# Kernel optimization log

Hardware: AMD Instinct MI355X
Metric: run time of the kernel (lower is better)

Reference implementation:

```python
import jax, jax.numpy as jnp
import numpy as np

B, T, D, H = 4096, 512, 8, 64  # batch, seq_len, input_size, hidden_size


def setup_inputs() -> dict:
    key = jax.random.key(0)
    ks = jax.random.split(key, 11)
    s = lambda k, shape: (jax.random.normal(k, shape, dtype=jnp.float32) * 0.1)
    return {
        "x": jax.random.normal(ks[0], (B, T, D), dtype=jnp.float32),
        # layer 0 (input_size -> H), PyTorch gate order i,f,g,o packed along 4H
        "Wih0": s(ks[1], (4 * H, D)),
        "Whh0": s(ks[2], (4 * H, H)),
        "bih0": s(ks[3], (4 * H,)),
        "bhh0": s(ks[4], (4 * H,)),
        # layer 1 (H -> H)
        "Wih1": s(ks[5], (4 * H, H)),
        "Whh1": s(ks[6], (4 * H, H)),
        "bih1": s(ks[7], (4 * H,)),
        "bhh1": s(ks[8], (4 * H,)),
        # final linear head H -> 1
        "Wfc": s(ks[9], (1, H)),
        "bfc": s(ks[10], (1,)),
    }


def _lstm_layer(x, Wih, Whh, bih, bhh):
    """Single-direction LSTM layer over x:[B,T,Din] -> hs:[B,T,H]."""
    b, t, _ = x.shape
    h_dim = Whh.shape[1]
    # Precompute input contribution for all timesteps (one big GEMM).
    xg = jnp.einsum("btd,gd->btg", x, Wih) + bih + bhh  # [B,T,4H]

    def step(carry, gx_t):
        h, c = carry
        z = gx_t + h @ Whh.T  # [B,4H]
        i, f, g, o = jnp.split(z, 4, axis=-1)
        i = jax.nn.sigmoid(i)
        f = jax.nn.sigmoid(f)
        g = jnp.tanh(g)
        o = jax.nn.sigmoid(o)
        c = f * c + i * g
        h = o * jnp.tanh(c)
        return (h, c), h

    h0 = jnp.zeros((b, h_dim), x.dtype)
    c0 = jnp.zeros((b, h_dim), x.dtype)
    (_, _), hs = jax.lax.scan(step, (h0, c0), jnp.swapaxes(xg, 0, 1))
    return jnp.swapaxes(hs, 0, 1)  # [B,T,H]


def reference(x, Wih0, Whh0, bih0, bhh0, Wih1, Whh1, bih1, bhh1, Wfc, bfc):
    # nn.LSTM with num_layers=2, batch_first=True; dropout inactive in eval.
    h1 = _lstm_layer(x, Wih0, Whh0, bih0, bhh0)
    h2 = _lstm_layer(h1, Wih1, Whh1, bih1, bhh1)
    last = h2[:, -1, :]  # [B,H]
    return last @ Wfc.T + bfc  # [B,1]
```

## Files before the change

### kernel.cpp

```cpp
#include <hip/hip_runtime.h>

#define BTOT 4096
#define TB   512
#define BD   8
#define BSL  16

#define A0TOG  2048
#define A1BASE 4096
#define A1TOG  1024
#define XBASE  6144
#define XTOG   8192
#define NLDS   22528

typedef __attribute__((ext_vector_type(8))) short  short8;
typedef __attribute__((ext_vector_type(4))) float  f32x4;

static __device__ __forceinline__ unsigned short f2bf(float f) {
    unsigned u = __float_as_uint(f);
    u += 0x7fffu + ((u >> 16) & 1u);
    return (unsigned short)(u >> 16);
}
static __device__ __forceinline__ float bf2f(unsigned short h) {
    return __uint_as_float(((unsigned)h) << 16);
}
static __device__ __forceinline__ unsigned pkbf(float a, float b) {
    unsigned r;
    asm("v_cvt_pk_bf16_f32 %0, %1, %2" : "=v"(r) : "v"(a), "v"(b));
    return r;
}

static __device__ __forceinline__ void inv8(const float d[8], float v[8]) {
    const float p0 = d[0]*d[1], p1 = d[2]*d[3], p2 = d[4]*d[5], p3 = d[6]*d[7];
    const float q0 = p0*p1, q1 = p2*p3;
    const float r  = __builtin_amdgcn_rcpf(q0*q1);
    const float iq0 = q1*r,  iq1 = q0*r;
    const float ip0 = p1*iq0, ip1 = p0*iq0, ip2 = p3*iq1, ip3 = p2*iq1;
    v[0]=d[1]*ip0; v[1]=d[0]*ip0; v[2]=d[3]*ip1; v[3]=d[2]*ip1;
    v[4]=d[5]*ip2; v[5]=d[4]*ip2; v[6]=d[7]*ip3; v[7]=d[6]*ip3;
}
static __device__ __forceinline__ void inv4(const float d[4], float v[4]) {
    const float p0 = d[0]*d[1], p1 = d[2]*d[3];
    const float r  = __builtin_amdgcn_rcpf(p0*p1);
    const float ip0 = p1*r, ip1 = p0*r;
    v[0]=d[1]*ip0; v[1]=d[0]*ip0; v[2]=d[3]*ip1; v[3]=d[2]*ip1;
}

static __device__ __forceinline__ void gates4(
    const f32x4 ai, const f32x4 af, const f32x4 ag, const f32x4 ao,
    float cc[4], unsigned hp[2])
{
    float ei[4], ef[4], eg[4], eo[4];
    #pragma unroll
    for (int r = 0; r < 4; ++r) {
        ei[r] = __builtin_amdgcn_exp2f(ai[r]);
        ef[r] = __builtin_amdgcn_exp2f(af[r]);
        eg[r] = __builtin_amdgcn_exp2f(ag[r]);
        eo[r] = __builtin_amdgcn_exp2f(ao[r]);
    }
    const float d01[8] = {1.f+ei[0],1.f+ef[0],1.f+eg[0],1.f+eo[0],
                          1.f+ei[1],1.f+ef[1],1.f+eg[1],1.f+eo[1]};
    const float d23[8] = {1.f+ei[2],1.f+ef[2],1.f+eg[2],1.f+eo[2],
                          1.f+ei[3],1.f+ef[3],1.f+eg[3],1.f+eo[3]};
    float v01[8], v23[8];
    inv8(d01, v01); inv8(d23, v23);
    const float iv[4] = {v01[0], v01[4], v23[0], v23[4]};
    const float fv[4] = {v01[1], v01[5], v23[1], v23[5]};
    const float gd[4] = {v01[2], v01[6], v23[2], v23[6]};
    const float ov[4] = {v01[3], v01[7], v23[3], v23[7]};
    float nc[4], dc[4];
    #pragma unroll
    for (int r = 0; r < 4; ++r) {
        const float gv = (eg[r] - 1.f) * gd[r];
        cc[r] = fv[r] * cc[r] + iv[r] * gv;
        const float ec = __builtin_amdgcn_exp2f(2.88539008f * cc[r]);
        nc[r] = ec - 1.f; dc[r] = ec + 1.f;
    }
    float id[4];
    inv4(dc, id);
    const float h0 = ov[0]*(nc[0]*id[0]), h1 = ov[1]*(nc[1]*id[1]);
    const float h2 = ov[2]*(nc[2]*id[2]), h3 = ov[3]*(nc[3]*id[3]);
    hp[0] = pkbf(h0, h1); hp[1] = pkbf(h2, h3);
}

static __device__ __forceinline__ void stage_x(
    unsigned short* lds16, const float* __restrict__ x, int rb, int tid, int t0)
{
    const int buf = (t0 >> 6) & 1;
    const int row = tid >> 5, u = tid & 31;
    const float* gp = x + (size_t)(rb + row) * (TB * BD) + t0 * BD + u * 16;
    const float4 v0 = ((const float4*)gp)[0];
    const float4 v1 = ((const float4*)gp)[1];
    const float4 v2 = ((const float4*)gp)[2];
    const float4 v3 = ((const float4*)gp)[3];
    const int el = XBASE + buf * XTOG + (u * 2) * 128 + row * 8;
    uint4 s0, s1;
    s0.x = pkbf(v0.x, v0.y); s0.y = pkbf(v0.z, v0.w);
    s0.z = pkbf(v1.x, v1.y); s0.w = pkbf(v1.z, v1.w);
    s1.x = pkbf(v2.x, v2.y); s1.y = pkbf(v2.z, v2.w);
    s1.z = pkbf(v3.x, v3.y); s1.w = pkbf(v3.z, v3.w);
    *(uint4*)(lds16 + el)       = s0;
    *(uint4*)(lds16 + el + 128) = s1;
}

__global__ __launch_bounds__(512, 2) void lstm2_fused(
    const float* __restrict__ x,
    const float* __restrict__ Wih0, const float* __restrict__ Whh0,
    const float* __restrict__ bih0, const float* __restrict__ bhh0,
    const float* __restrict__ Wih1, const float* __restrict__ Whh1,
    const float* __restrict__ bih1, const float* __restrict__ bhh1,
    const float* __restrict__ Wfc,  const float* __restrict__ bfc,
    float* __restrict__ out)
{
    __shared__ __align__(16) unsigned short lds16[NLDS];

    const int tid  = threadIdx.x;
    const int wid  = tid >> 6;
    const int lane = tid & 63;
    const int q    = lane >> 4;
    const int ln   = lane & 15;
    const int rb   = blockIdx.x * BSL;

    const bool L1w = (wid >= 4);
    const int  g   = L1w ? (wid - 4) : wid;
    const int  jc  = g * 16 + ln;

    const float SCI = -1.44269504f;
    const float SCG =  2.88539008f;
    short8 Bf[4][4];
    #pragma unroll
    for (int G = 0; G < 4; ++G) {
        const int n = G * 64 + jc;
        const float sc = (G == 2) ? SCG : SCI;
        #pragma unroll
        for (int ki = 0; ki < 4; ++ki) {
            union { unsigned short u[8]; short8 v; } t;
            #pragma unroll
            for (int j = 0; j < 8; ++j) {
                const int k = ki * 32 + q * 8 + j;
                float wv = 0.0f;
                if (!L1w) {
                    if (ki < 3) {
                        if (k < 64)      wv = Whh0[n * 64 + k];
                        else if (k < 72) wv = Wih0[n * 8 + (k - 64)];
                    }
                } else {
                    if (k < 64)          wv = Wih1[n * 64 + k];
                    else                 wv = Whh1[n * 64 + (k - 64)];
                }
                t.u[j] = f2bf(sc * wv);
            }
            Bf[G][ki] = t.v;
        }
    }
    float bias[4];
    #pragma unroll
    for (int G = 0; G < 4; ++G) {
        const int n = G * 64 + jc;
        const float sc = (G == 2) ? SCG : SCI;
        bias[G] = sc * (L1w ? (bih1[n] + bhh1[n]) : (bih0[n] + bhh0[n]));
    }

    stage_x(lds16, x, rb, tid, 0);
    {
        unsigned* z = (unsigned*)lds16;
        #pragma unroll
        for (int i = 0; i < 6; ++i) z[tid + i * 512] = 0;
    }
    __syncthreads();
    if (tid < 16) {
        const uint4 v = *(const uint4*)(lds16 + XBASE + tid * 8);
        *(uint4*)(lds16 + 8 * 128 + tid * 8) = v;
    }
    __syncthreads();

    const int rbase = q * 128 + ln * 8;
    const int wb    = (jc >> 3) * 128 + q * 32 + (jc & 7);
    int rdA  = rbase;
    int wr0  = A0TOG + wb;
    int rdH0 = rbase;
    int rdH1 = A1BASE + rbase;
    int wrH1 = A1BASE + A1TOG + wb;
    int xw   = A0TOG + 1024 + lane * 8;

    float cc[4] = {0.f, 0.f, 0.f, 0.f};

    for (int it = 0; it <= TB; ++it) {
        if (((it & 63) == 62) && (it + 2 < TB))
            stage_x(lds16, x, rb, tid, it + 2);

        if (!L1w) {
            if (it < TB) {
                if (wid == 0 && lane < 16 && it + 1 < TB) {
                    const int tn = it + 1;
                    const int xr = XBASE + ((tn >> 6) & 1) * XTOG + (tn & 63) * 128 + lane * 8;
                    const uint4 v = *(const uint4*)(lds16 + xr);
                    *(uint4*)(lds16 + xw) = v;
                }
                const short8 a0 = *(const short8*)(lds16 + rdA);
                const short8 a1 = *(const short8*)(lds16 + rdA + 512);
                const short8 a2 = *(const short8*)(lds16 + rdA + 1024);

                f32x4 ai = {bias[0], bias[0], bias[0], bias[0]};
                f32x4 af = {bias[1], bias[1], bias[1], bias[1]};
                f32x4 ag = {bias[2], bias[2], bias[2], bias[2]};
                f32x4 ao = {bias[3], bias[3], bias[3], bias[3]};
                ai = __builtin_amdgcn_mfma_f32_16x16x32_bf16(a0, Bf[0][0], ai, 0, 0, 0);
                af = __builtin_amdgcn_mfma_f32_16x16x32_bf16(a0, Bf[1][0], af, 0, 0, 0);
                ag = __builtin_amdgcn_mfma_f32_16x16x32_bf16(a0, Bf[2][0], ag, 0, 0, 0);
                ao = __builtin_amdgcn_mfma_f32_16x16x32_bf16(a0, Bf[3][0], ao, 0, 0, 0);
                ai = __builtin_amdgcn_mfma_f32_16x16x32_bf16(a1, Bf[0][1], ai, 0, 0, 0);
                af = __builtin_amdgcn_mfma_f32_16x16x32_bf16(a1, Bf[1][1], af, 0, 0, 0);
                ag = __builtin_amdgcn_mfma_f32_16x16x32_bf16(a1, Bf[2][1], ag, 0, 0, 0);
                ao = __builtin_amdgcn_mfma_f32_16x16x32_bf16(a1, Bf[3][1], ao, 0, 0, 0);
                ai = __builtin_amdgcn_mfma_f32_16x16x32_bf16(a2, Bf[0][2], ai, 0, 0, 0);
                af = __builtin_amdgcn_mfma_f32_16x16x32_bf16(a2, Bf[1][2], af, 0, 0, 0);
                ag = __builtin_amdgcn_mfma_f32_16x16x32_bf16(a2, Bf[2][2], ag, 0, 0, 0);
                ao = __builtin_amdgcn_mfma_f32_16x16x32_bf16(a2, Bf[3][2], ao, 0, 0, 0);

                unsigned hp[2];
                gates4(ai, af, ag, ao, cc, hp);
                lds16[wr0]           = (unsigned short)hp[0];
                lds16[wr0 + 8]       = (unsigned short)(hp[0] >> 16);
                lds16[wr0 + 16]      = (unsigned short)hp[1];
                lds16[wr0 + 24]      = (unsigned short)(hp[1] >> 16);
            }
        } else {
            if (it >= 1) {
                const short8 a0 = *(const short8*)(lds16 + rdH0);
                const short8 a1 = *(const short8*)(lds16 + rdH0 + 512);
                const short8 a2 = *(const short8*)(lds16 + rdH1);
                const short8 a3 = *(const short8*)(lds16 + rdH1 + 512);

                f32x4 ai = {bias[0], bias[0], bias[0], bias[0]};
                f32x4 af = {bias[1], bias[1], bias[1], bias[1]};
                f32x4 ag = {bias[2], bias[2], bias[2], bias[2]};
                f32x4 ao = {bias[3], bias[3], bias[3], bias[3]};
                ai = __builtin_amdgcn_mfma_f32_16x16x32_bf16(a0, Bf[0][0], ai, 0, 0, 0);
                af = __builtin_amdgcn_mfma_f32_16x16x32_bf16(a0, Bf[1][0], af, 0, 0, 0);
                ag = __builtin_amdgcn_mfma_f32_16x16x32_bf16(a0, Bf[2][0], ag, 0, 0, 0);
                ao = __builtin_amdgcn_mfma_f32_16x16x32_bf16(a0, Bf[3][0], ao, 0, 0, 0);
                ai = __builtin_amdgcn_mfma_f32_16x16x32_bf16(a1, Bf[0][1], ai, 0, 0, 0);
                af = __builtin_amdgcn_mfma_f32_16x16x32_bf16(a1, Bf[1][1], af, 0, 0, 0);
                ag = __builtin_amdgcn_mfma_f32_16x16x32_bf16(a1, Bf[2][1], ag, 0, 0, 0);
                ao = __builtin_amdgcn_mfma_f32_16x16x32_bf16(a1, Bf[3][1], ao, 0, 0, 0);
                ai = __builtin_amdgcn_mfma_f32_16x16x32_bf16(a2, Bf[0][2], ai, 0, 0, 0);
                af = __builtin_amdgcn_mfma_f32_16x16x32_bf16(a2, Bf[1][2], af, 0, 0, 0);
                ag = __builtin_amdgcn_mfma_f32_16x16x32_bf16(a2, Bf[2][2], ag, 0, 0, 0);
                ao = __builtin_amdgcn_mfma_f32_16x16x32_bf16(a2, Bf[3][2], ao, 0, 0, 0);
                ai = __builtin_amdgcn_mfma_f32_16x16x32_bf16(a3, Bf[0][3], ai, 0, 0, 0);
                af = __builtin_amdgcn_mfma_f32_16x16x32_bf16(a3, Bf[1][3], af, 0, 0, 0);
                ag = __builtin_amdgcn_mfma_f32_16x16x32_bf16(a3, Bf[2][3], ag, 0, 0, 0);
                ao = __builtin_amdgcn_mfma_f32_16x16x32_bf16(a3, Bf[3][3], ao, 0, 0, 0);

                unsigned hp[2];
                gates4(ai, af, ag, ao, cc, hp);
                lds16[wrH1]          = (unsigned short)hp[0];
                lds16[wrH1 + 8]      = (unsigned short)(hp[0] >> 16);
                lds16[wrH1 + 16]     = (unsigned short)hp[1];
                lds16[wrH1 + 24]     = (unsigned short)(hp[1] >> 16);
            }
        }
        __syncthreads();
        rdA ^= A0TOG; wr0 ^= A0TOG; rdH0 ^= A0TOG; xw ^= A0TOG;
        rdH1 ^= A1TOG; wrH1 ^= A1TOG;
    }

    if (tid < BSL) {
        float s = bfc[0];
        #pragma unroll 8
        for (int j = 0; j < 64; ++j)
            s += bf2f(lds16[A1BASE + A1TOG + (j >> 3) * 128 + tid * 8 + (j & 7)]) * Wfc[j];
        out[rb + tid] = s;
    }
}

extern "C" void kernel_launch(void* const* d_in, const int* in_sizes, int n_in,
                              void* d_out, int out_size, void* d_ws, size_t ws_size,
                              hipStream_t stream) {
    const float* x    = (const float*)d_in[0];
    const float* Wih0 = (const float*)d_in[1];
    const float* Whh0 = (const float*)d_in[2];
    const float* bih0 = (const float*)d_in[3];
    const float* bhh0 = (const float*)d_in[4];
    const float* Wih1 = (const float*)d_in[5];
    const float* Whh1 = (const float*)d_in[6];
    const float* bih1 = (const float*)d_in[7];
    const float* bhh1 = (const float*)d_in[8];
    const float* Wfc  = (const float*)d_in[9];
    const float* bfc  = (const float*)d_in[10];
    float* out = (float*)d_out;

    dim3 grid(BTOT / BSL);
    dim3 block(512);
    lstm2_fused<<<grid, block, 0, stream>>>(x, Wih0, Whh0, bih0, bhh0,
                                            Wih1, Whh1, bih1, bhh1, Wfc, bfc, out);
}
```

Measured before the change: 604.7 us.

## Halve batch rows per block, read x directly from LDS, simplify gate math

Cuts the batch slice per block from 16 to 8 rows, which doubles the grid and raises launch_bounds occupancy to 4 blocks per CU. The LDS layout is rebuilt to match, and the per-step copy of x into the A-operand buffer is dropped in favour of an MFMA operand read straight from the staged x buffer. Gate activations now use one reciprocal per sigmoid or tanh instead of the batched product-inverse trick. Half of each 16-row MFMA tile is now wasted on duplicated rows. The gate path issues more rcp instructions in exchange for fewer multiplies, and the x staging loads are narrower.

Measured after the change: 791.9 us. 31.0% more time.

```diff
diff --git a/kernel.cpp b/kernel.cpp
--- a/kernel.cpp
+++ b/kernel.cpp
@@ -3,14 +3,13 @@
 #define BTOT 4096
 #define TB   512
 #define BD   8
-#define BSL  16
-
-#define A0TOG  2048
-#define A1BASE 4096
+#define BSL  8
+
+#define A0TOG  1024
+#define A1BASE 2048
 #define A1TOG  1024
-#define XBASE  6144
-#define XTOG   8192
-#define NLDS   22528
+#define XBASE  4096
+#define NLDS   20480
 
 typedef __attribute__((ext_vector_type(8))) short  short8;
 typedef __attribute__((ext_vector_type(4))) float  f32x4;
@@ -29,80 +28,39 @@
     return r;
 }
 
-static __device__ __forceinline__ void inv8(const float d[8], float v[8]) {
-    const float p0 = d[0]*d[1], p1 = d[2]*d[3], p2 = d[4]*d[5], p3 = d[6]*d[7];
-    const float q0 = p0*p1, q1 = p2*p3;
-    const float r  = __builtin_amdgcn_rcpf(q0*q1);
-    const float iq0 = q1*r,  iq1 = q0*r;
-    const float ip0 = p1*iq0, ip1 = p0*iq0, ip2 = p3*iq1, ip3 = p2*iq1;
-    v[0]=d[1]*ip0; v[1]=d[0]*ip0; v[2]=d[3]*ip1; v[3]=d[2]*ip1;
-    v[4]=d[5]*ip2; v[5]=d[4]*ip2; v[6]=d[7]*ip3; v[7]=d[6]*ip3;
-}
-static __device__ __forceinline__ void inv4(const float d[4], float v[4]) {
-    const float p0 = d[0]*d[1], p1 = d[2]*d[3];
-    const float r  = __builtin_amdgcn_rcpf(p0*p1);
-    const float ip0 = p1*r, ip1 = p0*r;
-    v[0]=d[1]*ip0; v[1]=d[0]*ip0; v[2]=d[3]*ip1; v[3]=d[2]*ip1;
-}
-
 static __device__ __forceinline__ void gates4(
     const f32x4 ai, const f32x4 af, const f32x4 ag, const f32x4 ao,
     float cc[4], unsigned hp[2])
 {
-    float ei[4], ef[4], eg[4], eo[4];
+    float h[4];
     #pragma unroll
     for (int r = 0; r < 4; ++r) {
-        ei[r] = __builtin_amdgcn_exp2f(ai[r]);
-        ef[r] = __builtin_amdgcn_exp2f(af[r]);
-        eg[r] = __builtin_amdgcn_exp2f(ag[r]);
-        eo[r] = __builtin_amdgcn_exp2f(ao[r]);
-    }
-    const float d01[8] = {1.f+ei[0],1.f+ef[0],1.f+eg[0],1.f+eo[0],
-                          1.f+ei[1],1.f+ef[1],1.f+eg[1],1.f+eo[1]};
-    const float d23[8] = {1.f+ei[2],1.f+ef[2],1.f+eg[2],1.f+eo[2],
-                          1.f+ei[3],1.f+ef[3],1.f+eg[3],1.f+eo[3]};
-    float v01[8], v23[8];
-    inv8(d01, v01); inv8(d23, v23);
-    const float iv[4] = {v01[0], v01[4], v23[0], v23[4]};
-    const float fv[4] = {v01[1], v01[5], v23[1], v23[5]};
-    const float gd[4] = {v01[2], v01[6], v23[2], v23[6]};
-    const float ov[4] = {v01[3], v01[7], v23[3], v23[7]};
-    float nc[4], dc[4];
-    #pragma unroll
-    for (int r = 0; r < 4; ++r) {
-        const float gv = (eg[r] - 1.f) * gd[r];
-        cc[r] = fv[r] * cc[r] + iv[r] * gv;
+        const float iv = __builtin_amdgcn_rcpf(1.f + __builtin_amdgcn_exp2f(ai[r]));
+        const float fv = __builtin_amdgcn_rcpf(1.f + __builtin_amdgcn_exp2f(af[r]));
+        const float gv = 1.f - 2.f * __builtin_amdgcn_rcpf(1.f + __builtin_amdgcn_exp2f(ag[r]));
+        const float ov = __builtin_amdgcn_rcpf(1.f + __builtin_amdgcn_exp2f(ao[r]));
+        cc[r] = fv * cc[r] + iv * gv;
         const float ec = __builtin_amdgcn_exp2f(2.88539008f * cc[r]);
-        nc[r] = ec - 1.f; dc[r] = ec + 1.f;
-    }
-    float id[4];
-    inv4(dc, id);
-    const float h0 = ov[0]*(nc[0]*id[0]), h1 = ov[1]*(nc[1]*id[1]);
-    const float h2 = ov[2]*(nc[2]*id[2]), h3 = ov[3]*(nc[3]*id[3]);
-    hp[0] = pkbf(h0, h1); hp[1] = pkbf(h2, h3);
-}
-
-static __device__ __forceinline__ void stage_x(
+        h[r] = ov * (1.f - 2.f * __builtin_amdgcn_rcpf(1.f + ec));
+    }
+    hp[0] = pkbf(h[0], h[1]); hp[1] = pkbf(h[2], h[3]);
+}
+
+static __device__ __forceinline__ void stage_x8(
     unsigned short* lds16, const float* __restrict__ x, int rb, int tid, int t0)
 {
     const int buf = (t0 >> 6) & 1;
-    const int row = tid >> 5, u = tid & 31;
-    const float* gp = x + (size_t)(rb + row) * (TB * BD) + t0 * BD + u * 16;
+    const int tt = tid >> 3, row = tid & 7;
+    const float* gp = x + (size_t)(rb + row) * (TB * BD) + (t0 + tt) * BD;
     const float4 v0 = ((const float4*)gp)[0];
     const float4 v1 = ((const float4*)gp)[1];
-    const float4 v2 = ((const float4*)gp)[2];
-    const float4 v3 = ((const float4*)gp)[3];
-    const int el = XBASE + buf * XTOG + (u * 2) * 128 + row * 8;
-    uint4 s0, s1;
-    s0.x = pkbf(v0.x, v0.y); s0.y = pkbf(v0.z, v0.w);
-    s0.z = pkbf(v1.x, v1.y); s0.w = pkbf(v1.z, v1.w);
-    s1.x = pkbf(v2.x, v2.y); s1.y = pkbf(v2.z, v2.w);
-    s1.z = pkbf(v3.x, v3.y); s1.w = pkbf(v3.z, v3.w);
-    *(uint4*)(lds16 + el)       = s0;
-    *(uint4*)(lds16 + el + 128) = s1;
-}
-
-__global__ __launch_bounds__(512, 2) void lstm2_fused(
+    uint4 s;
+    s.x = pkbf(v0.x, v0.y); s.y = pkbf(v0.z, v0.w);
+    s.z = pkbf(v1.x, v1.y); s.w = pkbf(v1.z, v1.w);
+    *(uint4*)(lds16 + XBASE + buf * 8192 + tt * 128 + row * 8) = s;
+}
+
+__global__ __launch_bounds__(512, 4) void lstm2_fused(
     const float* __restrict__ x,
     const float* __restrict__ Wih0, const float* __restrict__ Whh0,
     const float* __restrict__ bih0, const float* __restrict__ bhh0,
@@ -160,45 +118,35 @@
         bias[G] = sc * (L1w ? (bih1[n] + bhh1[n]) : (bih0[n] + bhh0[n]));
     }
 
-    stage_x(lds16, x, rb, tid, 0);
     {
         unsigned* z = (unsigned*)lds16;
         #pragma unroll
-        for (int i = 0; i < 6; ++i) z[tid + i * 512] = 0;
+        for (int i = 0; i < 20; ++i) z[tid + i * 512] = 0;
     }
     __syncthreads();
-    if (tid < 16) {
-        const uint4 v = *(const uint4*)(lds16 + XBASE + tid * 8);
-        *(uint4*)(lds16 + 8 * 128 + tid * 8) = v;
-    }
+    stage_x8(lds16, x, rb, tid, 0);
     __syncthreads();
 
     const int rbase = q * 128 + ln * 8;
     const int wb    = (jc >> 3) * 128 + q * 32 + (jc & 7);
+    const int rsel  = (q == 0) ? ln : (8 + (ln & 7));
     int rdA  = rbase;
     int wr0  = A0TOG + wb;
     int rdH0 = rbase;
     int rdH1 = A1BASE + rbase;
     int wrH1 = A1BASE + A1TOG + wb;
-    int xw   = A0TOG + 1024 + lane * 8;
 
     float cc[4] = {0.f, 0.f, 0.f, 0.f};
 
     for (int it = 0; it <= TB; ++it) {
         if (((it & 63) == 62) && (it + 2 < TB))
-            stage_x(lds16, x, rb, tid, it + 2);
+            stage_x8(lds16, x, rb, tid, it + 2);
 
         if (!L1w) {
             if (it < TB) {
-                if (wid == 0 && lane < 16 && it + 1 < TB) {
-                    const int tn = it + 1;
-                    const int xr = XBASE + ((tn >> 6) & 1) * XTOG + (tn & 63) * 128 + lane * 8;
-                    const uint4 v = *(const uint4*)(lds16 + xr);
-                    *(uint4*)(lds16 + xw) = v;
-                }
                 const short8 a0 = *(const short8*)(lds16 + rdA);
                 const short8 a1 = *(const short8*)(lds16 + rdA + 512);
-                const short8 a2 = *(const short8*)(lds16 + rdA + 1024);
+                const short8 a2 = *(const short8*)(lds16 + XBASE + ((it & 127) << 7) + (rsel << 3));
 
                 f32x4 ai = {bias[0], bias[0], bias[0], bias[0]};
                 f32x4 af = {bias[1], bias[1], bias[1], bias[1]};
@@ -219,10 +167,10 @@
 
                 unsigned hp[2];
                 gates4(ai, af, ag, ao, cc, hp);
-                lds16[wr0]           = (unsigned short)hp[0];
-                lds16[wr0 + 8]       = (unsigned short)(hp[0] >> 16);
-                lds16[wr0 + 16]      = (unsigned short)hp[1];
-                lds16[wr0 + 24]      = (unsigned short)(hp[1] >> 16);
+                lds16[wr0]      = (unsigned short)hp[0];
+                lds16[wr0 + 8]  = (unsigned short)(hp[0] >> 16);
+                lds16[wr0 + 16] = (unsigned short)hp[1];
+                lds16[wr0 + 24] = (unsigned short)(hp[1] >> 16);
             }
         } else {
             if (it >= 1) {
@@ -254,14 +202,14 @@
 
                 unsigned hp[2];
                 gates4(ai, af, ag, ao, cc, hp);
-                lds16[wrH1]          = (unsigned short)hp[0];
-                lds16[wrH1 + 8]      = (unsigned short)(hp[0] >> 16);
-                lds16[wrH1 + 16]     = (unsigned short)hp[1];
-                lds16[wrH1 + 24]     = (unsigned short)(hp[1] >> 16);
+                lds16[wrH1]      = (unsigned short)hp[0];
+                lds16[wrH1 + 8]  = (unsigned short)(hp[0] >> 16);
+                lds16[wrH1 + 16] = (unsigned short)hp[1];
+                lds16[wrH1 + 24] = (unsigned short)(hp[1] >> 16);
             }
         }
         __syncthreads();
-        rdA ^= A0TOG; wr0 ^= A0TOG; rdH0 ^= A0TOG; xw ^= A0TOG;
+        rdA ^= A0TOG; wr0 ^= A0TOG; rdH0 ^= A0TOG;
         rdH1 ^= A1TOG; wrH1 ^= A1TOG;
     }
 
```
